# Kernel tuning notes

Hardware: AMD Instinct MI355X
Metric: run time of the kernel (lower is better)

Reference implementation:

```python
import jax, jax.numpy as jnp
import numpy as np

N = 50000      # nodes
DEG = 16       # avg degree
E = N * DEG    # edges
FIN = 128
FQK = 64
FV = 64
H = 8


def setup_inputs() -> dict:
    key = jax.random.key(0)
    k1, k2, k3, k4 = jax.random.split(key, 4)
    x = jax.random.normal(k1, (N, FIN), dtype=jnp.float32)
    # torch Linear(Fin, 2*Fqk+Fv, bias=False); stored here as [Fin, Ftot] so y = x @ W
    W = jax.random.normal(k2, (FIN, 2 * FQK + FV), dtype=jnp.float32) / np.sqrt(FIN)
    # edges: src sorted and covering all nodes (required by scatter_softmax semantics)
    src = jnp.repeat(jnp.arange(N, dtype=jnp.int32), DEG)
    dest = jax.random.randint(k3, (E,), 0, N, dtype=jnp.int32)
    ei = jnp.stack([src, dest])  # [2, E]
    batch = jnp.sort(jax.random.randint(k4, (N,), 0, 64, dtype=jnp.int32))
    return {"x": x, "W": W, "batch": batch, "ei": ei}


def reference(x, W, batch, ei):
    n = x.shape[0]
    Fh = FQK // H   # per-head qk dim
    Fhv = FV // H   # per-head v dim
    scaling = float(Fh) ** (-0.5)

    qkv = x @ W  # [N, 2*Fqk+Fv]
    q, k, v = jnp.split(qkv, [FQK, 2 * FQK], axis=-1)
    q = (q * scaling).reshape(n, H, Fh)
    k = k.reshape(n, H, Fh)
    v = v.reshape(n, H, Fhv)

    src, dest = ei[0], ei[1]
    qs = q[src]   # [E, H, Fh]
    ks = k[dest]  # [E, H, Fh]
    vs = v[dest]  # [E, H, Fhv]

    aw = jnp.einsum("ehf,ehf->eh", qs, ks)  # per-edge per-head logits

    # segment softmax over src (numerically stable, same math as exp/segsum(exp))
    amax = jax.ops.segment_max(aw, src, num_segments=n)
    ex = jnp.exp(aw - amax[src])
    denom = jax.ops.segment_sum(ex, src, num_segments=n)
    aw = ex / denom[src]  # [E, H]

    out = jax.ops.segment_sum(aw[:, :, None] * vs, src, num_segments=n)  # [N, H, Fhv]
    return out.reshape(n, H * Fhv)
```

## Files before the change

kernel.cpp:

```cpp
#include <hip/hip_runtime.h>
#include <math.h>

#define N_NODES 50000
#define DEG 16
#define E_EDGES (N_NODES * DEG)
#define FIN 128
#define FTOT 192
#define FQK 64
#define FV 64
#define H 8

typedef __attribute__((ext_vector_type(8))) short short8;
typedef __attribute__((ext_vector_type(4))) float float4v;

__device__ inline unsigned short f2bf(float f) {
    unsigned int u = __float_as_uint(f);
    unsigned int r = u + 0x7fffu + ((u >> 16) & 1u);
    return (unsigned short)(r >> 16);
}
__device__ inline float bf2f(unsigned short b) {
    return __uint_as_float(((unsigned int)b) << 16);
}

#define LDB 136
#define LDC 194

__global__ __launch_bounds__(256) void gemm_qkv(const float* __restrict__ x,
                                                const float* __restrict__ W,
                                                unsigned short* __restrict__ qkv) {
    __shared__ unsigned short Bt[FTOT * LDB];
    unsigned short* Ct = Bt;
    const int tid = threadIdx.x;

#pragma unroll
    for (int i = 0; i < 12; i++) {
        int idx = tid + i * 256;
        int n = idx % 192, kg = idx / 192;
        int k0 = kg * 8;
        unsigned short tmp[8];
#pragma unroll
        for (int j = 0; j < 8; j++)
            tmp[j] = f2bf(W[(k0 + j) * FTOT + n]);
        *(uint4*)(&Bt[n * LDB + k0]) = *(const uint4*)tmp;
    }

    const int wave = tid >> 6, lane = tid & 63;
    const int m = lane & 15, q = lane >> 4;
    const int row = blockIdx.x * 64 + wave * 16 + m;
    const int rowc = min(row, N_NODES - 1);

    short8 a[4];
    const float* xr = x + rowc * FIN;
#pragma unroll
    for (int s = 0; s < 4; s++) {
        float4v f0 = *(const float4v*)(xr + s * 32 + q * 8);
        float4v f1 = *(const float4v*)(xr + s * 32 + q * 8 + 4);
        short8 av;
        av[0] = (short)f2bf(f0.x); av[1] = (short)f2bf(f0.y);
        av[2] = (short)f2bf(f0.z); av[3] = (short)f2bf(f0.w);
        av[4] = (short)f2bf(f1.x); av[5] = (short)f2bf(f1.y);
        av[6] = (short)f2bf(f1.z); av[7] = (short)f2bf(f1.w);
        a[s] = av;
    }
    __syncthreads();

    float4v acc[12];
#pragma unroll
    for (int ct = 0; ct < 12; ct++) acc[ct] = (float4v){0.f, 0.f, 0.f, 0.f};
#pragma unroll
    for (int ct = 0; ct < 12; ct++) {
#pragma unroll
        for (int s = 0; s < 4; s++) {
            short8 b = *(const short8*)(&Bt[(ct * 16 + m) * LDB + s * 32 + q * 8]);
            acc[ct] = __builtin_amdgcn_mfma_f32_16x16x32_bf16(a[s], b, acc[ct], 0, 0, 0);
        }
    }
    __syncthreads();

    const int lrow0 = wave * 16 + q * 4;
#pragma unroll
    for (int ct = 0; ct < 12; ct++) {
        const int col = ct * 16 + m;
        int off; float scale;
        if (col < FQK)          { off = col;                      scale = 0.35355339059327373f; }
        else if (col < 2 * FQK) { off = 64 + 2 * (col - 64);      scale = 1.f; }
        else                    { off = 64 + 2 * (col - 128) + 1; scale = 1.f; }
#pragma unroll
        for (int i = 0; i < 4; i++)
            Ct[(lrow0 + i) * LDC + off] = f2bf(acc[ct][i] * scale);
    }
    __syncthreads();

    unsigned int* qg = (unsigned int*)qkv;
    const int base = blockIdx.x * 64;
#pragma unroll
    for (int i = 0; i < 24; i++) {
        int l = tid + i * 256;
        int r = l / 96, dw = l - r * 96;
        if (base + r < N_NODES)
            qg[(size_t)(base + r) * 96 + dw] = *(const unsigned int*)(&Ct[r * LDC + 2 * dw]);
    }
}

__global__ __launch_bounds__(256) void attn(const unsigned short* __restrict__ qkv,
                                            const int* __restrict__ dest,
                                            float* __restrict__ out) {
    const int node = blockIdx.x * 4 + (threadIdx.x >> 6);
    const int lane = threadIdx.x & 63;
    const int half = lane >> 5;
    const int l = lane & 31;
    if (node >= N_NODES) return;

    const unsigned int qw = *(const unsigned int*)(qkv + node * FTOT + 2 * l);
    const float q0 = __uint_as_float(qw << 16);
    const float q1 = __uint_as_float(qw & 0xffff0000u);
    const int dj = dest[node * DEG + (lane & 15)];

    uint2 kv[8];
#pragma unroll
    for (int t = 0; t < 8; t++) {
        const int d = __shfl(dj, 2 * t + half, 64);
        kv[t] = *(const uint2*)(qkv + d * FTOT + 64 + 4 * l);
    }

    float lg[8];
#pragma unroll
    for (int t = 0; t < 8; t++) {
        const float k0 = __uint_as_float(kv[t].x << 16);
        const float k1 = __uint_as_float(kv[t].y << 16);
        float p = fmaf(q0, k0, q1 * k1);
        p += __shfl_xor(p, 1, 64);
        p += __shfl_xor(p, 2, 64);
        lg[t] = p;
    }
    float mx = lg[0];
#pragma unroll
    for (int t = 1; t < 8; t++) mx = fmaxf(mx, lg[t]);
    float s = 0.f, o0 = 0.f, o1 = 0.f;
#pragma unroll
    for (int t = 0; t < 8; t++) {
        const float p = __expf(lg[t] - mx);
        s += p;
        o0 = fmaf(p, __uint_as_float(kv[t].x & 0xffff0000u), o0);
        o1 = fmaf(p, __uint_as_float(kv[t].y & 0xffff0000u), o1);
    }
    const float mo = __shfl_xor(mx, 32, 64);
    const float mn = fmaxf(mx, mo);
    const float f = __expf(mx - mn);
    s *= f; o0 *= f; o1 *= f;
    s  += __shfl_xor(s, 32, 64);
    o0 += __shfl_xor(o0, 32, 64);
    o1 += __shfl_xor(o1, 32, 64);
    if (half == 0) {
        float2 r; r.x = o0 / s; r.y = o1 / s;
        *(float2*)(out + node * 64 + 2 * l) = r;
    }
}

extern "C" void kernel_launch(void* const* d_in, const int* in_sizes, int n_in,
                              void* d_out, int out_size, void* d_ws, size_t ws_size,
                              hipStream_t stream) {
    const float* x = (const float*)d_in[0];
    const float* W = (const float*)d_in[1];
    const int* ei = (const int*)d_in[3];
    const int* dest = ei + E_EDGES;
    float* out = (float*)d_out;

    unsigned short* qkv = (unsigned short*)d_ws;

    gemm_qkv<<<(N_NODES + 63) / 64, 256, 0, stream>>>(x, W, qkv);
    attn<<<(N_NODES + 3) / 4, 256, 0, stream>>>(qkv, dest, out);
}
```

Before: 113.4 us.

## Pre-convert W to bf16, swizzle LDS B tile, remap attention lanes per edge

Adds a small kernel that converts and transposes W to bf16 once, so each GEMM block copies a pre-converted tile into LDS with an XOR swizzle instead of doing strided fp32 loads and conversions. This removes per-block W conversion work and LDS bank conflicts. The attention kernel is restructured so each group of 4 lanes owns one edge and loads that edge's full k/v row with wide 16-byte loads. Reductions then use cross-lane shuffles with a butterfly transpose for the output. The cost is an extra kernel launch and more shuffle traffic in the attention kernel.

Result: slower. 168.2 us (+48.3%).

```diff
diff --git a/kernel.cpp b/kernel.cpp
--- a/kernel.cpp
+++ b/kernel.cpp
@@ -18,39 +18,33 @@
     unsigned int r = u + 0x7fffu + ((u >> 16) & 1u);
     return (unsigned short)(r >> 16);
 }
-__device__ inline float bf2f(unsigned short b) {
-    return __uint_as_float(((unsigned int)b) << 16);
+
+#define LDC 194
+
+__global__ __launch_bounds__(256) void wprep(const float* __restrict__ W,
+                                             unsigned short* __restrict__ Wb) {
+    const int t = blockIdx.x * 256 + threadIdx.x;
+    const int n = t % 192, kg = t / 192;
+    unsigned short tmp[8];
+#pragma unroll
+    for (int j = 0; j < 8; j++)
+        tmp[j] = f2bf(W[(kg * 8 + j) * FTOT + n]);
+    *(uint4*)(Wb + n * FIN + kg * 8) = *(const uint4*)tmp;
 }
 
-#define LDB 136
-#define LDC 194
-
 __global__ __launch_bounds__(256) void gemm_qkv(const float* __restrict__ x,
-                                                const float* __restrict__ W,
+                                                const unsigned short* __restrict__ Wb,
                                                 unsigned short* __restrict__ qkv) {
-    __shared__ unsigned short Bt[FTOT * LDB];
+    __shared__ unsigned short Bt[FTOT * FIN];
     unsigned short* Ct = Bt;
     const int tid = threadIdx.x;
-
-#pragma unroll
-    for (int i = 0; i < 12; i++) {
-        int idx = tid + i * 256;
-        int n = idx % 192, kg = idx / 192;
-        int k0 = kg * 8;
-        unsigned short tmp[8];
-#pragma unroll
-        for (int j = 0; j < 8; j++)
-            tmp[j] = f2bf(W[(k0 + j) * FTOT + n]);
-        *(uint4*)(&Bt[n * LDB + k0]) = *(const uint4*)tmp;
-    }
-
     const int wave = tid >> 6, lane = tid & 63;
     const int m = lane & 15, q = lane >> 4;
     const int row = blockIdx.x * 64 + wave * 16 + m;
     const int rowc = min(row, N_NODES - 1);
 
     short8 a[4];
-    const float* xr = x + rowc * FIN;
+    const float* xr = x + (size_t)rowc * FIN;
 #pragma unroll
     for (int s = 0; s < 4; s++) {
         float4v f0 = *(const float4v*)(xr + s * 32 + q * 8);
@@ -62,6 +56,14 @@
         av[6] = (short)f2bf(f1.z); av[7] = (short)f2bf(f1.w);
         a[s] = av;
     }
+
+#pragma unroll
+    for (int i = 0; i < 12; i++) {
+        const int c = i * 256 + tid;
+        uint4 v = *(const uint4*)(Wb + c * 8);
+        const int cs = c ^ ((c >> 4) & 7);
+        *(uint4*)(&Bt[cs * 8]) = v;
+    }
     __syncthreads();
 
     float4v acc[12];
@@ -69,9 +71,12 @@
     for (int ct = 0; ct < 12; ct++) acc[ct] = (float4v){0.f, 0.f, 0.f, 0.f};
 #pragma unroll
     for (int ct = 0; ct < 12; ct++) {
+        const int n = ct * 16 + m;
+        const int sw = (n & 7) << 4;
 #pragma unroll
         for (int s = 0; s < 4; s++) {
-            short8 b = *(const short8*)(&Bt[(ct * 16 + m) * LDB + s * 32 + q * 8]);
+            const short8 b = *(const short8*)((const char*)Bt +
+                             (((n << 8) + s * 64 + q * 16) ^ sw));
             acc[ct] = __builtin_amdgcn_mfma_f32_16x16x32_bf16(a[s], b, acc[ct], 0, 0, 0);
         }
     }
@@ -107,54 +112,70 @@
                                             float* __restrict__ out) {
     const int node = blockIdx.x * 4 + (threadIdx.x >> 6);
     const int lane = threadIdx.x & 63;
-    const int half = lane >> 5;
-    const int l = lane & 31;
+    const int g = lane >> 2;
+    const int r = lane & 3;
     if (node >= N_NODES) return;
 
-    const unsigned int qw = *(const unsigned int*)(qkv + node * FTOT + 2 * l);
-    const float q0 = __uint_as_float(qw << 16);
-    const float q1 = __uint_as_float(qw & 0xffff0000u);
-    const int dj = dest[node * DEG + (lane & 15)];
+    const int d = dest[node * DEG + g];
 
-    uint2 kv[8];
+    const unsigned short* qp = qkv + (size_t)node * FTOT + 16 * r;
+    const uint4 qv0 = *(const uint4*)(qp);
+    const uint4 qv1 = *(const uint4*)(qp + 8);
+
+    const unsigned short* kp = qkv + (size_t)d * FTOT + 64 + 32 * r;
+    const uint4 kv0 = *(const uint4*)(kp);
+    const uint4 kv1 = *(const uint4*)(kp + 8);
+    const uint4 kv2 = *(const uint4*)(kp + 16);
+    const uint4 kv3 = *(const uint4*)(kp + 24);
+
+    const unsigned int qw[8]  = {qv0.x, qv0.y, qv0.z, qv0.w, qv1.x, qv1.y, qv1.z, qv1.w};
+    const unsigned int kvw[16] = {kv0.x, kv0.y, kv0.z, kv0.w, kv1.x, kv1.y, kv1.z, kv1.w,
+                                  kv2.x, kv2.y, kv2.z, kv2.w, kv3.x, kv3.y, kv3.z, kv3.w};
+
+    float la = 0.f, lb = 0.f;
 #pragma unroll
-    for (int t = 0; t < 8; t++) {
-        const int d = __shfl(dj, 2 * t + half, 64);
-        kv[t] = *(const uint2*)(qkv + d * FTOT + 64 + 4 * l);
+    for (int f = 0; f < 8; f++) {
+        const unsigned int qa = qw[f >> 1];
+        const unsigned int qb = qw[(f + 8) >> 1];
+        const float qfa = __uint_as_float((f & 1) ? (qa & 0xffff0000u) : (qa << 16));
+        const float qfb = __uint_as_float((f & 1) ? (qb & 0xffff0000u) : (qb << 16));
+        la = fmaf(qfa, __uint_as_float(kvw[f] << 16), la);
+        lb = fmaf(qfb, __uint_as_float(kvw[f + 8] << 16), lb);
     }
 
-    float lg[8];
+    float ma = la, mb = lb;
 #pragma unroll
-    for (int t = 0; t < 8; t++) {
-        const float k0 = __uint_as_float(kv[t].x << 16);
-        const float k1 = __uint_as_float(kv[t].y << 16);
-        float p = fmaf(q0, k0, q1 * k1);
-        p += __shfl_xor(p, 1, 64);
-        p += __shfl_xor(p, 2, 64);
-        lg[t] = p;
+    for (int msk = 4; msk <= 32; msk <<= 1) {
+        ma = fmaxf(ma, __shfl_xor(ma, msk, 64));
+        mb = fmaxf(mb, __shfl_xor(mb, msk, 64));
     }
-    float mx = lg[0];
+    const float pa = __expf(la - ma);
+    const float pb = __expf(lb - mb);
+    float sa = pa, sb = pb;
 #pragma unroll
-    for (int t = 1; t < 8; t++) mx = fmaxf(mx, lg[t]);
-    float s = 0.f, o0 = 0.f, o1 = 0.f;
+    for (int msk = 4; msk <= 32; msk <<= 1) {
+        sa += __shfl_xor(sa, msk, 64);
+        sb += __shfl_xor(sb, msk, 64);
+    }
+
+    float o[16];
 #pragma unroll
-    for (int t = 0; t < 8; t++) {
-        const float p = __expf(lg[t] - mx);
-        s += p;
-        o0 = fmaf(p, __uint_as_float(kv[t].x & 0xffff0000u), o0);
-        o1 = fmaf(p, __uint_as_float(kv[t].y & 0xffff0000u), o1);
+    for (int w = 0; w < 8; w++) {
+        o[w]     = pa * __uint_as_float(kvw[w] & 0xffff0000u);
+        o[w + 8] = pb * __uint_as_float(kvw[w + 8] & 0xffff0000u);
     }
-    const float mo = __shfl_xor(mx, 32, 64);
-    const float mn = fmaxf(mx, mo);
-    const float f = __expf(mx - mn);
-    s *= f; o0 *= f; o1 *= f;
-    s  += __shfl_xor(s, 32, 64);
-    o0 += __shfl_xor(o0, 32, 64);
-    o1 += __shfl_xor(o1, 32, 64);
-    if (half == 0) {
-        float2 r; r.x = o0 / s; r.y = o1 / s;
-        *(float2*)(out + node * 64 + 2 * l) = r;
+#pragma unroll
+    for (int m2 = 4, h = 8; h >= 1; m2 <<= 1, h >>= 1) {
+        const bool up = (lane & m2) != 0;
+#pragma unroll
+        for (int j = 0; j < h; j++) {
+            const float send = up ? o[j] : o[j + h];
+            const float recv = __shfl_xor(send, m2, 64);
+            o[j] = (up ? o[j + h] : o[j]) + recv;
+        }
     }
+    const int w = ((g & 1) << 3) | ((g & 2) << 1) | ((g & 4) >> 1) | ((g & 8) >> 3);
+    out[(size_t)node * 64 + 16 * r + w] = o[0] / ((w < 8) ? sa : sb);
 }
 
 extern "C" void kernel_launch(void* const* d_in, const int* in_sizes, int n_in,
@@ -167,7 +188,9 @@
     float* out = (float*)d_out;
 
     unsigned short* qkv = (unsigned short*)d_ws;
+    unsigned short* Wb  = qkv + (size_t)N_NODES * FTOT;
 
-    gemm_qkv<<<(N_NODES + 63) / 64, 256, 0, stream>>>(x, W, qkv);
+    wprep<<<12, 256, 0, stream>>>(W, Wb);
+    gemm_qkv<<<(N_NODES + 63) / 64, 256, 0, stream>>>(x, Wb, qkv);
     attn<<<(N_NODES + 3) / 4, 256, 0, stream>>>(qkv, dest, out);
 }
```
